# Kernel tuning notes

Hardware: AMD Instinct MI355X
Metric: run time of the kernel (lower is better)

Reference implementation:

```python
import jax, jax.numpy as jnp
import numpy as np
import math

B, S, D, H = 4, 2048, 1024, 16
HD = D // H  # head dim = 64

def setup_inputs() -> dict:
    key = jax.random.key(0)
    ks = jax.random.split(key, 8)
    scale = 1.0 / math.sqrt(D)
    return {
        "hidden_states": jax.random.normal(ks[0], (B, S, D), jnp.float32),
        "attention_mask": jnp.zeros((B, 1, 1, S), jnp.float32),
        "Wq": jax.random.normal(ks[1], (D, D), jnp.float32) * scale,
        "bq": jnp.zeros((D,), jnp.float32),
        "Wk": jax.random.normal(ks[2], (D, D), jnp.float32) * scale,
        "bk": jnp.zeros((D,), jnp.float32),
        "Wv": jax.random.normal(ks[3], (D, D), jnp.float32) * scale,
        "bv": jnp.zeros((D,), jnp.float32),
    }

def _split_heads(x):
    # [B,S,D] -> [B,H,S,HD]
    return x.reshape(B, S, H, HD).transpose(0, 2, 1, 3)

def reference(hidden_states, attention_mask, Wq, bq, Wk, bk, Wv, bv):
    q = _split_heads(hidden_states @ Wq + bq)
    k = _split_heads(hidden_states @ Wk + bk)
    v = _split_heads(hidden_states @ Wv + bv)
    scores = jnp.einsum("bhqd,bhkd->bhqk", q, k) / math.sqrt(HD)
    scores = scores + attention_mask
    probs = jax.nn.softmax(scores, axis=-1)
    ctx = jnp.einsum("bhqk,bhkd->bhqd", probs, v)
    # [B,H,S,HD] -> [B,S,D]
    return ctx.transpose(0, 2, 1, 3).reshape(B, S, D)
```

## Files before the change

kernel.cpp:

```cpp
#include <hip/hip_runtime.h>
#include <hip/hip_bf16.h>
#include <stdint.h>

#define Bc 4
#define Sc 2048
#define Dc 1024
#define Hc 16
#define HDc 64

typedef __attribute__((ext_vector_type(8))) __bf16 bf16x8;
typedef __attribute__((ext_vector_type(4))) __bf16 bf16x4;
typedef __attribute__((ext_vector_type(4))) float f32x4;
typedef __attribute__((ext_vector_type(16))) float f32x16;
typedef __attribute__((ext_vector_type(2))) int i32x2_t;

__device__ __forceinline__ f32x4 mfma16(bf16x8 a, bf16x8 b, f32x4 c) {
  return __builtin_amdgcn_mfma_f32_16x16x32_bf16(a, b, c, 0, 0, 0);
}
__device__ __forceinline__ f32x16 mfma32(bf16x8 a, bf16x8 b, f32x16 c) {
  return __builtin_amdgcn_mfma_f32_32x32x16_bf16(a, b, c, 0, 0, 0);
}
__device__ __forceinline__ uint32_t cvtpk_bf16(float lo, float hi) {
  uint32_t r;
  asm("v_cvt_pk_bf16_f32 %0, %1, %2" : "=v"(r) : "v"(lo), "v"(hi));
  return r;
}
__device__ __forceinline__ void gload_lds16(const void* g, void* l) {
  __builtin_amdgcn_global_load_lds(
      (const __attribute__((address_space(1))) void*)g,
      (__attribute__((address_space(3))) void*)l, 16, 0, 0);
}

__global__ __launch_bounds__(256) void hs2bf_kernel(const float* __restrict__ hs,
                                                    __bf16* __restrict__ Ah) {
  const size_t i = ((size_t)blockIdx.x * 256 + threadIdx.x) * 8;
  float4 f0 = *(const float4*)(hs + i);
  float4 f1 = *(const float4*)(hs + i + 4);
  bf16x8 o;
  o[0] = (__bf16)f0.x; o[1] = (__bf16)f0.y; o[2] = (__bf16)f0.z; o[3] = (__bf16)f0.w;
  o[4] = (__bf16)f1.x; o[5] = (__bf16)f1.y; o[6] = (__bf16)f1.z; o[7] = (__bf16)f1.w;
  *(bf16x8*)(Ah + i) = o;
}

__global__ __launch_bounds__(256) void wtrans_kernel(
    const float* __restrict__ Wq, const float* __restrict__ Wk,
    const float* __restrict__ Wv, __bf16* __restrict__ Wt) {
  const float* W = (blockIdx.z == 0) ? Wq : (blockIdx.z == 1 ? Wk : Wv);
  __bf16* out = Wt + (size_t)blockIdx.z * Dc * Dc;
  const int n0 = blockIdx.x * 64, k0 = blockIdx.y * 64;
  __shared__ float tile[64][65];
  const int tid = threadIdx.x;
  const int r = tid >> 2, cs = (tid & 3) * 16;
  const float* src = W + (size_t)(k0 + r) * Dc + n0 + cs;
  float4 f0 = *(const float4*)(src + 0);
  float4 f1 = *(const float4*)(src + 4);
  float4 f2 = *(const float4*)(src + 8);
  float4 f3 = *(const float4*)(src + 12);
#pragma unroll
  for (int j = 0; j < 4; ++j) {
    tile[r][cs + j] = ((const float*)&f0)[j];
    tile[r][cs + 4 + j] = ((const float*)&f1)[j];
    tile[r][cs + 8 + j] = ((const float*)&f2)[j];
    tile[r][cs + 12 + j] = ((const float*)&f3)[j];
  }
  __syncthreads();
  bf16x8 o0, o1;
#pragma unroll
  for (int j = 0; j < 8; ++j) {
    o0[j] = (__bf16)tile[cs + j][r];
    o1[j] = (__bf16)tile[cs + 8 + j][r];
  }
  __bf16* dst = out + (size_t)(n0 + r) * Dc + k0 + cs;
  *(bf16x8*)(dst) = o0;
  *(bf16x8*)(dst + 8) = o1;
}

__global__ __launch_bounds__(256) void qkv_gemm_kernel(
    const __bf16* __restrict__ A, const __bf16* __restrict__ Wt,
    const float* __restrict__ bq, const float* __restrict__ bk,
    const float* __restrict__ bv,
    __bf16* __restrict__ Qo, __bf16* __restrict__ Ko, __bf16* __restrict__ Vt) {
  const int orig = blockIdx.x;
  const int nt = orig & 7;
  const int rest = orig >> 3;
  const int w = rest >> 6;
  const int mt = rest & 63;
  const int m0 = mt * 128, n0 = nt * 128;

  const __bf16* Bp = Wt + (size_t)w * Dc * Dc;
  const float* bias = (w == 0) ? bq : (w == 1 ? bk : bv);

  __shared__ __attribute__((aligned(16))) __bf16 Asm[2][128 * 32];
  __shared__ __attribute__((aligned(16))) __bf16 Bsm[2][128 * 32];

  const int tid = threadIdx.x, lane = tid & 63, wid = tid >> 6;
  const int wm = wid >> 1, wn = wid & 1;
  const int lg = lane >> 4, li = lane & 15;

  f32x4 acc[4][4] = {};

  auto stage = [&](int buf, int k0) {
#pragma unroll
    for (int i = 0; i < 2; ++i) {
      const int u = i * 256 + tid;
      const int row = u >> 2, c = u & 3;
      const int gc = c ^ (row & 3);
      gload_lds16(A + (size_t)(m0 + row) * Dc + k0 + gc * 8,
                  &Asm[buf][i * 2048 + wid * 512]);
      gload_lds16(Bp + (size_t)(n0 + row) * Dc + k0 + gc * 8,
                  &Bsm[buf][i * 2048 + wid * 512]);
    }
  };

  int cur = 0;
  stage(0, 0);
  __syncthreads();

  for (int k0 = 0; k0 < Dc; k0 += 32) {
    if (k0 + 32 < Dc) stage(cur ^ 1, k0 + 32);
    bf16x8 af[4], bfr[4];
#pragma unroll
    for (int i = 0; i < 4; ++i) {
      const int rowa = wm * 64 + i * 16 + li;
      af[i] = *(const bf16x8*)&Asm[cur][rowa * 32 + (lg ^ (rowa & 3)) * 8];
      const int rowb = wn * 64 + i * 16 + li;
      bfr[i] = *(const bf16x8*)&Bsm[cur][rowb * 32 + (lg ^ (rowb & 3)) * 8];
    }
#pragma unroll
    for (int i = 0; i < 4; ++i)
#pragma unroll
      for (int j = 0; j < 4; ++j)
        acc[i][j] = mfma16(af[i], bfr[j], acc[i][j]);
    __syncthreads();
    cur ^= 1;
  }

  if (w < 2) {
    __bf16* out = (w == 0) ? Qo : Ko;
    const float scl = (w == 0) ? 0.125f : 1.0f;
#pragma unroll
    for (int i = 0; i < 4; ++i) {
#pragma unroll
      for (int j = 0; j < 4; ++j) {
        const int n = n0 + wn * 64 + j * 16 + li;
        const float bb = bias[n];
        const int h = n >> 6, hd = n & 63;
#pragma unroll
        for (int r = 0; r < 4; ++r) {
          const int m = m0 + wm * 64 + i * 16 + lg * 4 + r;
          const int b = m >> 11, s = m & 2047;
          out[(((size_t)b * Hc + h) * Sc + s) * HDc + hd] =
              (__bf16)((acc[i][j][r] + bb) * scl);
        }
      }
    }
  } else {
#pragma unroll
    for (int i = 0; i < 4; ++i) {
      const int mbase = m0 + wm * 64 + i * 16 + lg * 4;
      const int b = mbase >> 11, s0 = mbase & 2047;
#pragma unroll
      for (int j = 0; j < 4; ++j) {
        const int n = n0 + wn * 64 + j * 16 + li;
        const float bb = bias[n];
        const int h = n >> 6, hd = n & 63;
        bf16x4 o;
#pragma unroll
        for (int r = 0; r < 4; ++r) o[r] = (__bf16)(acc[i][j][r] + bb);
        *(bf16x4*)(Vt + (((size_t)b * Hc + h) * HDc + hd) * Sc + s0) = o;
      }
    }
  }
}

__global__ __launch_bounds__(256) void attn_kernel(
    const __bf16* __restrict__ Q, const __bf16* __restrict__ K,
    const __bf16* __restrict__ Vt, const float* __restrict__ mask,
    float* __restrict__ out) {
  const int qt = blockIdx.x;
  const int bh = blockIdx.y;
  const int b = bh >> 4, h = bh & 15;
  const __bf16* qb = Q + (size_t)bh * Sc * HDc;
  const __bf16* kb = K + (size_t)bh * Sc * HDc;
  const __bf16* vtb = Vt + (size_t)bh * HDc * Sc;
  const float* mk = mask + (size_t)b * Sc;

  const int tid = threadIdx.x, lane = tid & 63, wid = tid >> 6;
  const int hi = lane >> 5, qr = lane & 31;

  __shared__ __attribute__((aligned(16))) __bf16 Ksm[2][64 * 64];
  __shared__ __attribute__((aligned(16))) __bf16 Vsm[2][64 * 64];
  __shared__ __attribute__((aligned(16))) float Msm[2][64];

  const int q0 = qt * 128 + wid * 32;

  bf16x8 qf[4];
#pragma unroll
  for (int c = 0; c < 4; ++c)
    qf[c] = *(const bf16x8*)(qb + (size_t)(q0 + qr) * HDc + c * 16 + hi * 8);

  bf16x8 onesv;
#pragma unroll
  for (int j = 0; j < 8; ++j) onesv[j] = (__bf16)1.0f;

  f32x16 oacc[2] = {};
  f32x16 lacc = {};

  auto stage = [&](int buf, int kv0) {
#pragma unroll
    for (int i = 0; i < 2; ++i) {
      const int u = i * 256 + tid;
      const int row = u >> 3, c = u & 7;
      gload_lds16(kb + (size_t)(kv0 + row) * HDc + ((c ^ (row & 7)) * 8),
                  &Ksm[buf][i * 2048 + wid * 512]);
      gload_lds16(vtb + (size_t)row * Sc + kv0 + ((c ^ (row & 7)) * 8),
                  &Vsm[buf][i * 2048 + wid * 512]);
    }
    if (tid < 16) {
      float4 mv = *(const float4*)(mk + kv0 + tid * 4);
      *(float4*)&Msm[buf][tid * 4] = mv;
    }
  };

  auto body = [&](int buf) {
    f32x16 sacc[2];
#pragma unroll
    for (int kb2 = 0; kb2 < 2; ++kb2) {
#pragma unroll
      for (int g = 0; g < 4; ++g) {
        const float4 m4 = *(const float4*)&Msm[buf][kb2 * 32 + g * 8 + hi * 4];
#pragma unroll
        for (int e = 0; e < 4; ++e) sacc[kb2][g * 4 + e] = ((const float*)&m4)[e];
      }
    }
    __builtin_amdgcn_s_setprio(1);
#pragma unroll
    for (int kb2 = 0; kb2 < 2; ++kb2) {
      const int row = kb2 * 32 + qr;
#pragma unroll
      for (int c = 0; c < 4; ++c) {
        const bf16x8 kf =
            *(const bf16x8*)&Ksm[buf][row * 64 + (((2 * c + hi) ^ (row & 7)) * 8)];
        sacc[kb2] = mfma32(kf, qf[c], sacc[kb2]);
      }
    }
    __builtin_amdgcn_s_setprio(0);

    bf16x8 pa[4];
#pragma unroll
    for (int kb2 = 0; kb2 < 2; ++kb2) {
      uint32_t wv[8];
#pragma unroll
      for (int j = 0; j < 8; ++j)
        wv[j] = cvtpk_bf16(__expf(sacc[kb2][2 * j]), __expf(sacc[kb2][2 * j + 1]));
#pragma unroll
      for (int cc = 0; cc < 2; ++cc) {
        i32x2_t s02 = __builtin_amdgcn_permlane32_swap(
            (int)wv[cc * 4 + 0], (int)wv[cc * 4 + 2], false, false);
        i32x2_t s13 = __builtin_amdgcn_permlane32_swap(
            (int)wv[cc * 4 + 1], (int)wv[cc * 4 + 3], false, false);
        union { uint32_t u[4]; bf16x8 v; } af;
        af.u[0] = (uint32_t)s02[0];
        af.u[1] = (uint32_t)s13[0];
        af.u[2] = (uint32_t)s02[1];
        af.u[3] = (uint32_t)s13[1];
        pa[kb2 * 2 + cc] = af.v;
      }
    }

    __builtin_amdgcn_s_setprio(1);
#pragma unroll
    for (int kc = 0; kc < 4; ++kc) {
      lacc = mfma32(pa[kc], onesv, lacc);
#pragma unroll
      for (int nb = 0; nb < 2; ++nb) {
        const int hd = nb * 32 + qr;
        const bf16x8 vf =
            *(const bf16x8*)&Vsm[buf][hd * 64 + (((2 * kc + hi) ^ (hd & 7)) * 8)];
        oacc[nb] = mfma32(pa[kc], vf, oacc[nb]);
      }
    }
    __builtin_amdgcn_s_setprio(0);
    __syncthreads();
  };

  stage(0, 0);
  __syncthreads();

  const int NT = Sc / 64;
  for (int t = 0; t < NT; t += 2) {
    if (t + 1 < NT) stage(1, (t + 1) * 64);
    body(0);
    if (t + 2 < NT) stage(0, (t + 2) * 64);
    body(1);
  }

  float inv[16];
#pragma unroll
  for (int r = 0; r < 16; ++r) inv[r] = __builtin_amdgcn_rcpf(lacc[r]);
#pragma unroll
  for (int nb = 0; nb < 2; ++nb) {
#pragma unroll
    for (int r = 0; r < 16; ++r) {
      const int row = (r & 3) + 8 * (r >> 2) + 4 * hi;
      const int qg = q0 + row;
      out[((size_t)b * Sc + qg) * Dc + h * HDc + nb * 32 + qr] =
          oacc[nb][r] * inv[r];
    }
  }
}

extern "C" void kernel_launch(void* const* d_in, const int* in_sizes, int n_in,
                              void* d_out, int out_size, void* d_ws,
                              size_t ws_size, hipStream_t stream) {
  const float* hs = (const float*)d_in[0];
  const float* mask = (const float*)d_in[1];
  const float* Wq = (const float*)d_in[2];
  const float* bq = (const float*)d_in[3];
  const float* Wk = (const float*)d_in[4];
  const float* bk = (const float*)d_in[5];
  const float* Wv = (const float*)d_in[6];
  const float* bv = (const float*)d_in[7];
  float* out = (float*)d_out;

  char* ws = (char*)d_ws;
  const size_t qkv_bytes = (size_t)Bc * Hc * Sc * HDc * 2;
  __bf16* Wt = (__bf16*)ws;
  __bf16* Ah = (__bf16*)(ws + 6291456);
  __bf16* Q = (__bf16*)(ws + 6291456 + qkv_bytes);
  __bf16* K = (__bf16*)(ws + 6291456 + 2 * qkv_bytes);
  __bf16* Vt = (__bf16*)(ws + 6291456 + 3 * qkv_bytes);

  hs2bf_kernel<<<4096, 256, 0, stream>>>(hs, Ah);
  wtrans_kernel<<<dim3(16, 16, 3), 256, 0, stream>>>(Wq, Wk, Wv, Wt);
  qkv_gemm_kernel<<<1536, 256, 0, stream>>>(Ah, Wt, bq, bk, bv, Q, K, Vt);
  attn_kernel<<<dim3(16, 64), 256, 0, stream>>>(Q, K, Vt, mask, out);
}
```

Measured before the change: 208.4 us.

## Store K/V tiles in fragment-major LDS layout and use exp2 with prescaled log2e

K and V tiles are now staged into LDS in the exact per-lane MFMA fragment order, so each fragment read becomes a constant offset from a per-lane base instead of an XOR-swizzled address. This removes address arithmetic from the inner loop and may change bank-conflict behaviour. Separately, the Q scale and mask are premultiplied by log2(e), so the softmax exponent can use the hardware exp2 instruction directly in place of __expf. The global load pattern changes with the new staging and may coalesce less well.

Result: slower. 216.5 us (+3.9%).

```diff
diff --git a/kernel.cpp b/kernel.cpp
--- a/kernel.cpp
+++ b/kernel.cpp
@@ -7,6 +7,7 @@
 #define Dc 1024
 #define Hc 16
 #define HDc 64
+#define LOG2E 1.44269504088896f
 
 typedef __attribute__((ext_vector_type(8))) __bf16 bf16x8;
 typedef __attribute__((ext_vector_type(4))) __bf16 bf16x4;
@@ -137,7 +138,7 @@
 
   if (w < 2) {
     __bf16* out = (w == 0) ? Qo : Ko;
-    const float scl = (w == 0) ? 0.125f : 1.0f;
+    const float scl = (w == 0) ? (0.125f * LOG2E) : 1.0f;
 #pragma unroll
     for (int i = 0; i < 4; ++i) {
 #pragma unroll
@@ -209,20 +210,25 @@
   auto stage = [&](int buf, int kv0) {
 #pragma unroll
     for (int i = 0; i < 2; ++i) {
-      const int u = i * 256 + tid;
-      const int row = u >> 3, c = u & 7;
-      gload_lds16(kb + (size_t)(kv0 + row) * HDc + ((c ^ (row & 7)) * 8),
-                  &Ksm[buf][i * 2048 + wid * 512]);
-      gload_lds16(vtb + (size_t)row * Sc + kv0 + ((c ^ (row & 7)) * 8),
-                  &Vsm[buf][i * 2048 + wid * 512]);
+      const int s = i * 256 + tid;
+      const int sqr = s & 31, shi = (s >> 5) & 1;
+      gload_lds16(kb + (size_t)(kv0 + (s >> 8) * 32 + sqr) * HDc +
+                      ((s >> 6) & 3) * 16 + shi * 8,
+                  &Ksm[buf][(i * 256 + wid * 64) * 8]);
+      gload_lds16(vtb + (size_t)(((s >> 6) & 1) * 32 + sqr) * Sc + kv0 +
+                      (s >> 7) * 16 + shi * 8,
+                  &Vsm[buf][(i * 256 + wid * 64) * 8]);
     }
     if (tid < 16) {
       float4 mv = *(const float4*)(mk + kv0 + tid * 4);
+      mv.x *= LOG2E; mv.y *= LOG2E; mv.z *= LOG2E; mv.w *= LOG2E;
       *(float4*)&Msm[buf][tid * 4] = mv;
     }
   };
 
   auto body = [&](int buf) {
+    const __bf16* Kb = &Ksm[buf][lane * 8];
+    const __bf16* Vb = &Vsm[buf][lane * 8];
     f32x16 sacc[2];
 #pragma unroll
     for (int kb2 = 0; kb2 < 2; ++kb2) {
@@ -236,11 +242,9 @@
     __builtin_amdgcn_s_setprio(1);
 #pragma unroll
     for (int kb2 = 0; kb2 < 2; ++kb2) {
-      const int row = kb2 * 32 + qr;
 #pragma unroll
       for (int c = 0; c < 4; ++c) {
-        const bf16x8 kf =
-            *(const bf16x8*)&Ksm[buf][row * 64 + (((2 * c + hi) ^ (row & 7)) * 8)];
+        const bf16x8 kf = *(const bf16x8*)(Kb + (kb2 * 4 + c) * 512);
         sacc[kb2] = mfma32(kf, qf[c], sacc[kb2]);
       }
     }
@@ -252,7 +256,8 @@
       uint32_t wv[8];
 #pragma unroll
       for (int j = 0; j < 8; ++j)
-        wv[j] = cvtpk_bf16(__expf(sacc[kb2][2 * j]), __expf(sacc[kb2][2 * j + 1]));
+        wv[j] = cvtpk_bf16(__builtin_amdgcn_exp2f(sacc[kb2][2 * j]),
+                           __builtin_amdgcn_exp2f(sacc[kb2][2 * j + 1]));
 #pragma unroll
       for (int cc = 0; cc < 2; ++cc) {
         i32x2_t s02 = __builtin_amdgcn_permlane32_swap(
@@ -274,9 +279,7 @@
       lacc = mfma32(pa[kc], onesv, lacc);
 #pragma unroll
       for (int nb = 0; nb < 2; ++nb) {
-        const int hd = nb * 32 + qr;
-        const bf16x8 vf =
-            *(const bf16x8*)&Vsm[buf][hd * 64 + (((2 * kc + hi) ^ (hd & 7)) * 8)];
+        const bf16x8 vf = *(const bf16x8*)(Vb + (kc * 2 + nb) * 512);
         oacc[nb] = mfma32(pa[kc], vf, oacc[nb]);
       }
     }
```
